# Optimization experiments

Measured on AMD Instinct MI355X. Metric: run time of the kernel, lower is better.

Reference implementation:

```python
import jax, jax.numpy as jnp
import numpy as np
from jax import lax

B, T, E, D, A, C, FILT = 32, 1600, 1024, 1024, 512, 10, 100
SCALING = 2.0


def setup_inputs() -> dict:
    key = jax.random.key(0)
    ks = jax.random.split(key, 14)
    enc_hs_pad = jax.random.normal(ks[0], (B, T, E), dtype=jnp.float32)
    # lengths in [T//2, T] so every row has valid positions
    enc_hs_len = jax.random.randint(ks[1], (B,), T // 2, T + 1, dtype=jnp.int32)
    dec_z = jax.random.normal(ks[2], (B, D), dtype=jnp.float32)
    # previous attention weights: uniform over valid frames, normalized
    valid = (jnp.arange(T)[None, :] < enc_hs_len[:, None]).astype(jnp.float32)
    raw = jax.random.uniform(ks[3], (B, T), dtype=jnp.float32) * valid
    att_prev = raw / jnp.sum(raw, axis=1, keepdims=True)
    att_h = 0.1 * jax.random.normal(ks[4], (B, A), dtype=jnp.float32)
    att_c = 0.1 * jax.random.normal(ks[5], (B, A), dtype=jnp.float32)
    W_enc = jax.random.normal(ks[6], (A, E), dtype=jnp.float32) / np.sqrt(E)
    b_enc = jax.random.normal(ks[7], (A,), dtype=jnp.float32) * 0.01
    W_dec = jax.random.normal(ks[8], (A, D), dtype=jnp.float32) / np.sqrt(D)
    conv_w = jax.random.normal(ks[9], (C, 1, 2 * FILT + 1), dtype=jnp.float32) / np.sqrt(2 * FILT + 1)
    W_ih = jax.random.normal(ks[10], (4 * A, C), dtype=jnp.float32) / np.sqrt(C)
    W_hh = jax.random.normal(ks[11], (4 * A, A), dtype=jnp.float32) / np.sqrt(A)
    W_g = jax.random.normal(ks[12], (A,), dtype=jnp.float32) / np.sqrt(A)
    b_g = jnp.zeros((1,), dtype=jnp.float32)
    return {"enc_hs_pad": enc_hs_pad, "enc_hs_len": enc_hs_len, "dec_z": dec_z,
            "att_prev": att_prev, "att_h": att_h, "att_c": att_c,
            "W_enc": W_enc, "b_enc": b_enc, "W_dec": W_dec, "conv_w": conv_w,
            "W_ih": W_ih, "W_hh": W_hh, "W_g": W_g, "b_g": b_g}


def reference(enc_hs_pad, enc_hs_len, dec_z, att_prev, att_h, att_c,
              W_enc, b_enc, W_dec, conv_w, W_ih, W_hh, W_g, b_g):
    t_len = enc_hs_pad.shape[1]
    filts = (conv_w.shape[-1] - 1) // 2

    # precompute encoder projection (B, T, A)
    pre_enc = jnp.einsum('bte,ae->bta', enc_hs_pad, W_enc) + b_enc

    # location conv on previous attention: (B,1,T) -> (B,C,T), relu, global max-pool over T
    att_conv = lax.conv_general_dilated(att_prev[:, None, :], conv_w,
                                        window_strides=(1,), padding=[(filts, filts)],
                                        dimension_numbers=('NCH', 'OIH', 'NCH'))
    att_feat = jnp.max(jax.nn.relu(att_conv), axis=-1)  # (B, C)

    # LSTMCell (no bias), pytorch gate order i, f, g, o
    gates = att_feat @ W_ih.T + att_h @ W_hh.T  # (B, 4A)
    i, f, g, o = jnp.split(gates, 4, axis=-1)
    c_new = jax.nn.sigmoid(f) * att_c + jax.nn.sigmoid(i) * jnp.tanh(g)
    h_new = jax.nn.sigmoid(o) * jnp.tanh(c_new)  # (B, A)

    dec_proj = dec_z @ W_dec.T  # (B, A)
    # scores (B, T)
    e = jnp.tanh(h_new[:, None, :] + pre_enc + dec_proj[:, None, :]) @ W_g + b_g

    mask = jnp.arange(t_len)[None, :] >= enc_hs_len[:, None]  # True = pad
    e = jnp.where(mask, jnp.finfo(e.dtype).min, e)
    w = jax.nn.softmax(SCALING * e, axis=1)  # (B, T)

    ctx = jnp.einsum('bt,bte->be', w, enc_hs_pad)  # (B, E)
    return ctx, w, h_new, c_new
```

## Files before the change

kernel.cpp:

```cpp
#include <hip/hip_runtime.h>
#include <hip/hip_bf16.h>

#define BB 32
#define TT 1600
#define EE 1024
#define AA 512
#define CC 10
#define KW 201

typedef __attribute__((ext_vector_type(8))) short short8;
typedef __attribute__((ext_vector_type(4))) float f32x4;

__device__ __forceinline__ float sigm(float x) { return 1.f / (1.f + expf(-x)); }

__device__ __forceinline__ unsigned int cvt2(float a, float b) {
    float2 f2; f2.x = a; f2.y = b;
    __hip_bfloat162 h = __float22bfloat162_rn(f2);
    unsigned int r;
    __builtin_memcpy(&r, &h, 4);
    return r;
}

__device__ __forceinline__ void gl_lds16(const void* g, void* l) {
    __builtin_amdgcn_global_load_lds(
        (const __attribute__((address_space(1))) unsigned int*)g,
        (__attribute__((address_space(3))) unsigned int*)l, 16, 0, 0);
}

#define AF_OFF   0
#define R_OFF    320
#define E_OFF    16704
#define WBF_OFF  67904

#define CTX_OFF 0
#define W_OFF   32768
#define H_OFF   83968
#define C_OFF   100352

__global__ void prep_kernel(const float* __restrict__ att_prev,
                            const float* __restrict__ conv_w,
                            const float* __restrict__ W_enc,
                            float* __restrict__ af,
                            unsigned short* __restrict__ Wbf) {
    int bx = blockIdx.x, tid = threadIdx.x;
    if (bx >= 320) {
        int i = (bx - 320) * 256 + tid;
        float4 v = reinterpret_cast<const float4*>(W_enc)[i];
        uint2 p;
        p.x = cvt2(v.x, v.y);
        p.y = cvt2(v.z, v.w);
        reinterpret_cast<uint2*>(Wbf)[i] = p;
        return;
    }
    int b = bx / 10, c = bx % 10;
    __shared__ float xs[1808];
    __shared__ float wsm[KW];
    __shared__ float red[256];
    const float* xp = att_prev + b * TT;
    for (int i = tid; i < 1808; i += 256) {
        int g = i - 100;
        xs[i] = (g >= 0 && g < TT) ? xp[g] : 0.f;
    }
    if (tid < KW) wsm[tid] = conv_w[c * KW + tid];
    __syncthreads();
    float mx = 0.f;
    #pragma unroll 1
    for (int sweep = 0; sweep < 2; ++sweep) {
        int t0 = sweep * 1024 + tid * 4;
        if (t0 >= TT) break;
        float a0 = xs[t0], a1 = xs[t0 + 1], a2 = xs[t0 + 2], a3 = xs[t0 + 3];
        float s0 = 0.f, s1 = 0.f, s2 = 0.f, s3 = 0.f;
        #pragma unroll 4
        for (int k = 0; k < KW; ++k) {
            float w = wsm[k];
            s0 += w * a0; s1 += w * a1; s2 += w * a2; s3 += w * a3;
            a0 = a1; a1 = a2; a2 = a3;
            a3 = xs[t0 + k + 4];
        }
        mx = fmaxf(mx, fmaxf(fmaxf(s0, s1), fmaxf(s2, s3)));
    }
    red[tid] = mx; __syncthreads();
    for (int s = 128; s > 0; s >>= 1) {
        if (tid < s) red[tid] = fmaxf(red[tid], red[tid + s]);
        __syncthreads();
    }
    if (tid == 0) af[b * CC + c] = red[0];
}

__global__ void gates_lstm_kernel(const float* __restrict__ af,
                                  const float* __restrict__ att_h,
                                  const float* __restrict__ dec_z,
                                  const float* __restrict__ att_c,
                                  const float* __restrict__ W_ih,
                                  const float* __restrict__ W_hh,
                                  const float* __restrict__ W_dec,
                                  float* __restrict__ out,
                                  float* __restrict__ r_ws) {
    __shared__ float gsm[8][32];
    __shared__ float dsm[8][32];
    int tid = threadIdx.x;
    int a0 = blockIdx.x * 2;
    int b = tid & 31;
    if (tid < 256) {
        int u = tid >> 5;
        int gate = u >> 1, ai = u & 1;
        int j = gate * 512 + a0 + ai;
        float s = 0.f;
        #pragma unroll
        for (int k = 0; k < 10; ++k) s += af[b * 10 + k] * W_ih[j * 10 + k];
        const float4* wr = reinterpret_cast<const float4*>(W_hh + (size_t)j * 512);
        const float4* hr = reinterpret_cast<const float4*>(att_h + b * 512);
        #pragma unroll 4
        for (int k = 0; k < 128; ++k) {
            float4 w = wr[k], h = hr[k];
            s += w.x * h.x + w.y * h.y + w.z * h.z + w.w * h.w;
        }
        gsm[u][b] = s;
    } else {
        int v = (tid - 256) >> 5;
        int ai = v & 1, q = v >> 1;
        int a = a0 + ai;
        const float4* wr = reinterpret_cast<const float4*>(W_dec + (size_t)a * 1024) + q * 64;
        const float4* zr = reinterpret_cast<const float4*>(dec_z + (size_t)b * 1024) + q * 64;
        float s = 0.f;
        #pragma unroll 4
        for (int k = 0; k < 64; ++k) {
            float4 w = wr[k], z = zr[k];
            s += w.x * z.x + w.y * z.y + w.z * z.z + w.w * z.w;
        }
        dsm[v][b] = s;
    }
    __syncthreads();
    if (tid < 64) {
        int ai = tid >> 5;
        int a = a0 + ai;
        float ig = gsm[ai][b], fg = gsm[2 + ai][b], gg = gsm[4 + ai][b], og = gsm[6 + ai][b];
        float cn = sigm(fg) * att_c[b * 512 + a] + sigm(ig) * tanhf(gg);
        float hn = sigm(og) * tanhf(cn);
        out[H_OFF + b * 512 + a] = hn;
        out[C_OFF + b * 512 + a] = cn;
        float dec = dsm[ai][b] + dsm[2 + ai][b] + dsm[4 + ai][b] + dsm[6 + ai][b];
        r_ws[b * 512 + a] = hn + dec;
    }
}

__global__ void __launch_bounds__(1024, 4)
score_gemm_kernel(const float* __restrict__ enc,
                  const unsigned short* __restrict__ Wbf,
                  const float* __restrict__ b_enc,
                  const float* __restrict__ r_ws,
                  const float* __restrict__ W_g,
                  float* __restrict__ e_ws) {
    __shared__ __align__(16) short As[2][4096];
    __shared__ __align__(16) short Bs[2][8192];
    __shared__ float e_part[8][128];

    int tid = threadIdx.x;
    int lane = tid & 63, wv = tid >> 6;
    int wm = wv >> 3, wn = wv & 7;
    int col = lane & 15, quad = lane >> 4;
    int m0 = blockIdx.x * 128;

    const unsigned short* bsrc = Wbf + (size_t)((tid >> 6) * 16 + (tid & 15)) * EE
                                 + ((tid >> 4) & 3) * 8;
    int arow = tid >> 3, akq2 = tid & 7;
    const float* asrc = enc + (size_t)(m0 + arow) * EE + akq2 * 4;
    int adst = (arow >> 4) * 512 + ((akq2 >> 1) * 16 + (arow & 15)) * 8 + (akq2 & 1) * 4;

    f32x4 acc[4][2][2];
    #pragma unroll
    for (int mt = 0; mt < 4; ++mt)
        #pragma unroll
        for (int h = 0; h < 2; ++h)
            #pragma unroll
            for (int nt = 0; nt < 2; ++nt)
                acc[mt][h][nt] = (f32x4){0.f, 0.f, 0.f, 0.f};

    {
        gl_lds16(bsrc, &Bs[0][tid * 8]);
        float4 v = *reinterpret_cast<const float4*>(asrc);
        uint2 p; p.x = cvt2(v.x, v.y); p.y = cvt2(v.z, v.w);
        *reinterpret_cast<uint2*>(&As[0][adst]) = p;
    }
    __syncthreads();

    int bufA = 0;
    for (int k0 = 0; k0 < EE; k0 += 32) {
        bool last = (k0 == EE - 32);
        gl_lds16(bsrc + (size_t)256 * EE + k0, &Bs[1][tid * 8]);
        short8 a_frag[4];
        #pragma unroll
        for (int mt = 0; mt < 4; ++mt)
            a_frag[mt] = *reinterpret_cast<const short8*>(
                &As[bufA][(wm * 4 + mt) * 512 + (quad * 16 + col) * 8]);
        #pragma unroll
        for (int nt = 0; nt < 2; ++nt) {
            short8 bf = *reinterpret_cast<const short8*>(
                &Bs[0][(wn * 2 + nt) * 512 + (quad * 16 + col) * 8]);
            #pragma unroll
            for (int mt = 0; mt < 4; ++mt)
                acc[mt][0][nt] = __builtin_amdgcn_mfma_f32_16x16x32_bf16(
                    a_frag[mt], bf, acc[mt][0][nt], 0, 0, 0);
        }
        __syncthreads();
        float4 av;
        if (!last) {
            av = *reinterpret_cast<const float4*>(asrc + k0 + 32);
            gl_lds16(bsrc + k0 + 32, &Bs[0][tid * 8]);
        }
        #pragma unroll
        for (int nt = 0; nt < 2; ++nt) {
            short8 bf = *reinterpret_cast<const short8*>(
                &Bs[1][(wn * 2 + nt) * 512 + (quad * 16 + col) * 8]);
            #pragma unroll
            for (int mt = 0; mt < 4; ++mt)
                acc[mt][1][nt] = __builtin_amdgcn_mfma_f32_16x16x32_bf16(
                    a_frag[mt], bf, acc[mt][1][nt], 0, 0, 0);
        }
        if (!last) {
            uint2 p; p.x = cvt2(av.x, av.y); p.y = cvt2(av.z, av.w);
            *reinterpret_cast<uint2*>(&As[bufA ^ 1][adst]) = p;
        }
        __syncthreads();
        bufA ^= 1;
    }

    float wg[2][2], bn[2][2];
    #pragma unroll
    for (int h = 0; h < 2; ++h)
        #pragma unroll
        for (int nt = 0; nt < 2; ++nt) {
            int n = h * 256 + wn * 32 + nt * 16 + col;
            wg[h][nt] = W_g[n];
            bn[h][nt] = b_enc[n];
        }
    #pragma unroll
    for (int mt = 0; mt < 4; ++mt) {
        int mg = m0 + wm * 64 + mt * 16;
        int bb = mg / TT;
        float rr[2][2];
        #pragma unroll
        for (int h = 0; h < 2; ++h)
            #pragma unroll
            for (int nt = 0; nt < 2; ++nt)
                rr[h][nt] = r_ws[bb * AA + h * 256 + wn * 32 + nt * 16 + col];
        #pragma unroll
        for (int reg = 0; reg < 4; ++reg) {
            float p = 0.f;
            #pragma unroll
            for (int h = 0; h < 2; ++h)
                #pragma unroll
                for (int nt = 0; nt < 2; ++nt)
                    p += wg[h][nt] * tanhf(acc[mt][h][nt][reg] + bn[h][nt] + rr[h][nt]);
            p += __shfl_xor(p, 1);
            p += __shfl_xor(p, 2);
            p += __shfl_xor(p, 4);
            p += __shfl_xor(p, 8);
            if (col == 0) e_part[wn][wm * 64 + mt * 16 + quad * 4 + reg] = p;
        }
    }
    __syncthreads();
    if (tid < 128) {
        float s = 0.f;
        #pragma unroll
        for (int i = 0; i < 8; ++i) s += e_part[i][tid];
        e_ws[m0 + tid] = s;
    }
}

__global__ void ctx_softmax_kernel(const float* __restrict__ enc,
                                   const float* __restrict__ e_ws,
                                   const int* __restrict__ lens,
                                   float* __restrict__ w_out,
                                   float* __restrict__ ctx) {
    int b = blockIdx.x, ch = blockIdx.y;
    int tid = threadIdx.x;
    __shared__ float w_sm[1600];
    __shared__ float red[512];
    __shared__ float part[8][128];
    int len = lens[b];
    const float* e = e_ws + b * TT;
    float mx = -3.4e38f;
    for (int t = tid; t < len; t += 512) mx = fmaxf(mx, e[t]);
    red[tid] = mx; __syncthreads();
    for (int s = 256; s > 0; s >>= 1) {
        if (tid < s) red[tid] = fmaxf(red[tid], red[tid + s]);
        __syncthreads();
    }
    mx = red[0]; __syncthreads();
    float sum = 0.f;
    for (int t = tid; t < TT; t += 512) {
        float p = (t < len) ? expf(2.f * (e[t] - mx)) : 0.f;
        w_sm[t] = p; sum += p;
    }
    red[tid] = sum; __syncthreads();
    for (int s = 256; s > 0; s >>= 1) {
        if (tid < s) red[tid] += red[tid + s];
        __syncthreads();
    }
    float inv = 1.f / red[0];
    __syncthreads();
    for (int t = tid; t < TT; t += 512) {
        float wv = w_sm[t] * inv;
        w_sm[t] = wv;
        if (ch == 0) w_out[b * TT + t] = wv;
    }
    __syncthreads();
    int lane2 = tid & 63, w8 = tid >> 6;
    int tb = w8 * 200;
    const float* base = enc + (size_t)(b * TT + tb) * EE + ch * 128 + lane2 * 2;
    float cx = 0.f, cy = 0.f;
    #pragma unroll 1
    for (int i = 0; i < 200; i += 8) {
        #pragma unroll
        for (int j = 0; j < 8; ++j) {
            float2 v = *reinterpret_cast<const float2*>(base + (size_t)(i + j) * EE);
            float ww = w_sm[tb + i + j];
            cx += ww * v.x; cy += ww * v.y;
        }
    }
    part[w8][lane2 * 2] = cx;
    part[w8][lane2 * 2 + 1] = cy;
    __syncthreads();
    if (tid < 128) {
        float s = 0.f;
        #pragma unroll
        for (int i = 0; i < 8; ++i) s += part[i][tid];
        ctx[b * EE + ch * 128 + tid] = s;
    }
}

extern "C" void kernel_launch(void* const* d_in, const int* in_sizes, int n_in,
                              void* d_out, int out_size, void* d_ws, size_t ws_size,
                              hipStream_t stream) {
    const float* enc      = (const float*)d_in[0];
    const int*   lens     = (const int*)d_in[1];
    const float* dec_z    = (const float*)d_in[2];
    const float* att_prev = (const float*)d_in[3];
    const float* att_h    = (const float*)d_in[4];
    const float* att_c    = (const float*)d_in[5];
    const float* W_enc    = (const float*)d_in[6];
    const float* b_enc    = (const float*)d_in[7];
    const float* W_dec    = (const float*)d_in[8];
    const float* conv_w   = (const float*)d_in[9];
    const float* W_ih     = (const float*)d_in[10];
    const float* W_hh     = (const float*)d_in[11];
    const float* W_g      = (const float*)d_in[12];

    float* out = (float*)d_out;
    float* ws  = (float*)d_ws;
    float* af   = ws + AF_OFF;
    float* r_ws = ws + R_OFF;
    float* e_ws = ws + E_OFF;
    unsigned short* Wbf = (unsigned short*)(ws + WBF_OFF);

    prep_kernel<<<832, 256, 0, stream>>>(att_prev, conv_w, W_enc, af, Wbf);
    gates_lstm_kernel<<<256, 512, 0, stream>>>(af, att_h, dec_z, att_c,
                                               W_ih, W_hh, W_dec, out, r_ws);
    score_gemm_kernel<<<400, 1024, 0, stream>>>(enc, Wbf, b_enc, r_ws, W_g, e_ws);
    ctx_softmax_kernel<<<dim3(BB, 8), 512, 0, stream>>>(enc, e_ws, lens,
                                                        out + W_OFF, out + CTX_OFF);
}
```

Baseline: 494.4 us.

## Load W_enc fragments directly from global into registers, drop LDS B staging

The score GEMM no longer stages the bf16 W_enc tile in shared memory through global_load_lds. Each wave now reads its B fragments straight from global/L2 into registers, and only the A tile stays double-buffered in LDS. The loop is unrolled into explicit chunks that prefetch A two steps ahead, raise wave priority around the MFMA block, and use one barrier per step instead of two. This removes LDS traffic and a barrier per iteration, but W_enc is now re-read from cache by every wave, and any global latency is exposed to the MFMAs since B has no prefetch.

```diff
diff --git a/kernel.cpp b/kernel.cpp
--- a/kernel.cpp
+++ b/kernel.cpp
@@ -19,12 +19,6 @@
     unsigned int r;
     __builtin_memcpy(&r, &h, 4);
     return r;
-}
-
-__device__ __forceinline__ void gl_lds16(const void* g, void* l) {
-    __builtin_amdgcn_global_load_lds(
-        (const __attribute__((address_space(1))) unsigned int*)g,
-        (__attribute__((address_space(3))) unsigned int*)l, 16, 0, 0);
 }
 
 #define AF_OFF   0
@@ -152,7 +146,6 @@
                   const float* __restrict__ W_g,
                   float* __restrict__ e_ws) {
     __shared__ __align__(16) short As[2][4096];
-    __shared__ __align__(16) short Bs[2][8192];
     __shared__ float e_part[8][128];
 
     int tid = threadIdx.x;
@@ -161,11 +154,16 @@
     int col = lane & 15, quad = lane >> 4;
     int m0 = blockIdx.x * 128;
 
-    const unsigned short* bsrc = Wbf + (size_t)((tid >> 6) * 16 + (tid & 15)) * EE
-                                 + ((tid >> 4) & 3) * 8;
     int arow = tid >> 3, akq2 = tid & 7;
     const float* asrc = enc + (size_t)(m0 + arow) * EE + akq2 * 4;
     int adst = (arow >> 4) * 512 + ((akq2 >> 1) * 16 + (arow & 15)) * 8 + (akq2 & 1) * 4;
+
+    const unsigned short* bp[2][2];
+    #pragma unroll
+    for (int h = 0; h < 2; ++h)
+        #pragma unroll
+        for (int nt = 0; nt < 2; ++nt)
+            bp[h][nt] = Wbf + (size_t)(h * 256 + wn * 32 + nt * 16 + col) * EE + quad * 8;
 
     f32x4 acc[4][2][2];
     #pragma unroll
@@ -176,54 +174,65 @@
             for (int nt = 0; nt < 2; ++nt)
                 acc[mt][h][nt] = (f32x4){0.f, 0.f, 0.f, 0.f};
 
+    float4 av0, av1;
     {
-        gl_lds16(bsrc, &Bs[0][tid * 8]);
-        float4 v = *reinterpret_cast<const float4*>(asrc);
-        uint2 p; p.x = cvt2(v.x, v.y); p.y = cvt2(v.z, v.w);
-        *reinterpret_cast<uint2*>(&As[0][adst]) = p;
-    }
-    __syncthreads();
-
-    int bufA = 0;
-    for (int k0 = 0; k0 < EE; k0 += 32) {
-        bool last = (k0 == EE - 32);
-        gl_lds16(bsrc + (size_t)256 * EE + k0, &Bs[1][tid * 8]);
-        short8 a_frag[4];
-        #pragma unroll
-        for (int mt = 0; mt < 4; ++mt)
-            a_frag[mt] = *reinterpret_cast<const short8*>(
-                &As[bufA][(wm * 4 + mt) * 512 + (quad * 16 + col) * 8]);
-        #pragma unroll
-        for (int nt = 0; nt < 2; ++nt) {
-            short8 bf = *reinterpret_cast<const short8*>(
-                &Bs[0][(wn * 2 + nt) * 512 + (quad * 16 + col) * 8]);
-            #pragma unroll
-            for (int mt = 0; mt < 4; ++mt)
-                acc[mt][0][nt] = __builtin_amdgcn_mfma_f32_16x16x32_bf16(
-                    a_frag[mt], bf, acc[mt][0][nt], 0, 0, 0);
-        }
-        __syncthreads();
-        float4 av;
-        if (!last) {
-            av = *reinterpret_cast<const float4*>(asrc + k0 + 32);
-            gl_lds16(bsrc + k0 + 32, &Bs[0][tid * 8]);
-        }
-        #pragma unroll
-        for (int nt = 0; nt < 2; ++nt) {
-            short8 bf = *reinterpret_cast<const short8*>(
-                &Bs[1][(wn * 2 + nt) * 512 + (quad * 16 + col) * 8]);
-            #pragma unroll
-            for (int mt = 0; mt < 4; ++mt)
-                acc[mt][1][nt] = __builtin_amdgcn_mfma_f32_16x16x32_bf16(
-                    a_frag[mt], bf, acc[mt][1][nt], 0, 0, 0);
-        }
-        if (!last) {
-            uint2 p; p.x = cvt2(av.x, av.y); p.y = cvt2(av.z, av.w);
-            *reinterpret_cast<uint2*>(&As[bufA ^ 1][adst]) = p;
-        }
-        __syncthreads();
-        bufA ^= 1;
-    }
+        float4 p = *reinterpret_cast<const float4*>(asrc);
+        av1 = *reinterpret_cast<const float4*>(asrc + 32);
+        uint2 q; q.x = cvt2(p.x, p.y); q.y = cvt2(p.z, p.w);
+        *reinterpret_cast<uint2*>(&As[0][adst]) = q;
+        asm volatile("s_waitcnt lgkmcnt(0)\n\ts_barrier" ::: "memory");
+    }
+
+#define SCORE_CHUNK(RB, AVC, AVI, KC, PREF, WR)                                        \
+    {                                                                                  \
+        int k0 = (KC) * 32;                                                            \
+        short8 bf00 = *reinterpret_cast<const short8*>(bp[0][0] + k0);                 \
+        short8 bf01 = *reinterpret_cast<const short8*>(bp[0][1] + k0);                 \
+        short8 bf10 = *reinterpret_cast<const short8*>(bp[1][0] + k0);                 \
+        short8 bf11 = *reinterpret_cast<const short8*>(bp[1][1] + k0);                 \
+        if (PREF)                                                                      \
+            AVI = *reinterpret_cast<const float4*>(asrc + ((KC) + 2) * 32);            \
+        short8 af0 = *reinterpret_cast<const short8*>(                                 \
+            &As[RB][(wm * 4 + 0) * 512 + (quad * 16 + col) * 8]);                      \
+        short8 af1 = *reinterpret_cast<const short8*>(                                 \
+            &As[RB][(wm * 4 + 1) * 512 + (quad * 16 + col) * 8]);                      \
+        short8 af2 = *reinterpret_cast<const short8*>(                                 \
+            &As[RB][(wm * 4 + 2) * 512 + (quad * 16 + col) * 8]);                      \
+        short8 af3 = *reinterpret_cast<const short8*>(                                 \
+            &As[RB][(wm * 4 + 3) * 512 + (quad * 16 + col) * 8]);                      \
+        __builtin_amdgcn_s_setprio(1);                                                 \
+        acc[0][0][0] = __builtin_amdgcn_mfma_f32_16x16x32_bf16(af0, bf00, acc[0][0][0], 0, 0, 0); \
+        acc[0][0][1] = __builtin_amdgcn_mfma_f32_16x16x32_bf16(af0, bf01, acc[0][0][1], 0, 0, 0); \
+        acc[0][1][0] = __builtin_amdgcn_mfma_f32_16x16x32_bf16(af0, bf10, acc[0][1][0], 0, 0, 0); \
+        acc[0][1][1] = __builtin_amdgcn_mfma_f32_16x16x32_bf16(af0, bf11, acc[0][1][1], 0, 0, 0); \
+        acc[1][0][0] = __builtin_amdgcn_mfma_f32_16x16x32_bf16(af1, bf00, acc[1][0][0], 0, 0, 0); \
+        acc[1][0][1] = __builtin_amdgcn_mfma_f32_16x16x32_bf16(af1, bf01, acc[1][0][1], 0, 0, 0); \
+        acc[1][1][0] = __builtin_amdgcn_mfma_f32_16x16x32_bf16(af1, bf10, acc[1][1][0], 0, 0, 0); \
+        acc[1][1][1] = __builtin_amdgcn_mfma_f32_16x16x32_bf16(af1, bf11, acc[1][1][1], 0, 0, 0); \
+        acc[2][0][0] = __builtin_amdgcn_mfma_f32_16x16x32_bf16(af2, bf00, acc[2][0][0], 0, 0, 0); \
+        acc[2][0][1] = __builtin_amdgcn_mfma_f32_16x16x32_bf16(af2, bf01, acc[2][0][1], 0, 0, 0); \
+        acc[2][1][0] = __builtin_amdgcn_mfma_f32_16x16x32_bf16(af2, bf10, acc[2][1][0], 0, 0, 0); \
+        acc[2][1][1] = __builtin_amdgcn_mfma_f32_16x16x32_bf16(af2, bf11, acc[2][1][1], 0, 0, 0); \
+        acc[3][0][0] = __builtin_amdgcn_mfma_f32_16x16x32_bf16(af3, bf00, acc[3][0][0], 0, 0, 0); \
+        acc[3][0][1] = __builtin_amdgcn_mfma_f32_16x16x32_bf16(af3, bf01, acc[3][0][1], 0, 0, 0); \
+        acc[3][1][0] = __builtin_amdgcn_mfma_f32_16x16x32_bf16(af3, bf10, acc[3][1][0], 0, 0, 0); \
+        acc[3][1][1] = __builtin_amdgcn_mfma_f32_16x16x32_bf16(af3, bf11, acc[3][1][1], 0, 0, 0); \
+        __builtin_amdgcn_s_setprio(0);                                                 \
+        if (WR) {                                                                      \
+            uint2 q; q.x = cvt2(AVC.x, AVC.y); q.y = cvt2(AVC.z, AVC.w);               \
+            *reinterpret_cast<uint2*>(&As[(RB) ^ 1][adst]) = q;                        \
+        }                                                                              \
+        asm volatile("s_waitcnt lgkmcnt(0)\n\ts_barrier" ::: "memory");                \
+    }
+
+    #pragma unroll 1
+    for (int c = 0; c < 30; c += 2) {
+        SCORE_CHUNK(0, av1, av0, c, 1, 1)
+        SCORE_CHUNK(1, av0, av1, c + 1, 1, 1)
+    }
+    SCORE_CHUNK(0, av1, av0, 30, 0, 1)
+    SCORE_CHUNK(1, av0, av1, 31, 0, 0)
+#undef SCORE_CHUNK
 
     float wg[2][2], bn[2][2];
     #pragma unroll
```

After: 545.4 us. 10.3% more time.

## Triple-buffer score GEMM with async fp32 A loads into swizzled LDS

Applied to the files above, without the earlier changes.

Rewrites the score GEMM main loop as a three-stage pipeline. Both the fp32 encoder tile and the bf16 weight tile are fetched with asynchronous global-to-LDS loads, the A tile uses an XOR-swizzled layout, and fp32-to-bf16 conversion moves to the point where fragments are read. The loop computes both N halves per K chunk and uses explicit vmcnt waits plus s_setprio around the MFMA burst. This is meant to hide global load latency and cut the register staging and conversion work that sat on the critical path. The cost is about 144KB of LDS per block, which likely limits each CU to a single block.

```diff
diff --git a/kernel.cpp b/kernel.cpp
--- a/kernel.cpp
+++ b/kernel.cpp
@@ -151,8 +151,8 @@
                   const float* __restrict__ r_ws,
                   const float* __restrict__ W_g,
                   float* __restrict__ e_ws) {
-    __shared__ __align__(16) short As[2][4096];
-    __shared__ __align__(16) short Bs[2][8192];
+    __shared__ __align__(16) short Bs[3][16384];
+    __shared__ __align__(16) char  AsB[3][16384];
     __shared__ float e_part[8][128];
 
     int tid = threadIdx.x;
@@ -161,11 +161,22 @@
     int col = lane & 15, quad = lane >> 4;
     int m0 = blockIdx.x * 128;
 
-    const unsigned short* bsrc = Wbf + (size_t)((tid >> 6) * 16 + (tid & 15)) * EE
-                                 + ((tid >> 4) & 3) * 8;
-    int arow = tid >> 3, akq2 = tid & 7;
-    const float* asrc = enc + (size_t)(m0 + arow) * EE + akq2 * 4;
-    int adst = (arow >> 4) * 512 + ((akq2 >> 1) * 16 + (arow & 15)) * 8 + (akq2 & 1) * 4;
+    int agrp = tid >> 7;
+    int P = tid & 127;
+    int Lc = P ^ ((P >> 3) & 7);
+    int as_ = Lc >> 1, asub = Lc & 1;
+    int akoct = as_ >> 4, arowin = as_ & 15;
+    const float* asrc = enc + (size_t)(m0 + agrp * 16 + arowin) * EE + akoct * 8 + asub * 4;
+
+    int L0 = (quad * 16 + col) * 2;
+    int L1 = L0 + 1;
+    int p0 = (L0 ^ ((L0 >> 3) & 7)) * 16;
+    int p1 = (L1 ^ ((L1 >> 3) & 7)) * 16;
+
+    int bslot = tid & 63;
+    int boct = bslot >> 4, brow = bslot & 15;
+    const unsigned short* bsrc0 = Wbf + (size_t)((tid >> 6) * 16 + brow) * EE + boct * 8;
+    const unsigned short* bsrc1 = Wbf + (size_t)(((tid >> 6) + 16) * 16 + brow) * EE + boct * 8;
 
     f32x4 acc[4][2][2];
     #pragma unroll
@@ -176,63 +187,74 @@
             for (int nt = 0; nt < 2; ++nt)
                 acc[mt][h][nt] = (f32x4){0.f, 0.f, 0.f, 0.f};
 
-    {
-        gl_lds16(bsrc, &Bs[0][tid * 8]);
-        float4 v = *reinterpret_cast<const float4*>(asrc);
-        uint2 p; p.x = cvt2(v.x, v.y); p.y = cvt2(v.z, v.w);
-        *reinterpret_cast<uint2*>(&As[0][adst]) = p;
-    }
-    __syncthreads();
-
-    int bufA = 0;
-    for (int k0 = 0; k0 < EE; k0 += 32) {
-        bool last = (k0 == EE - 32);
-        gl_lds16(bsrc + (size_t)256 * EE + k0, &Bs[1][tid * 8]);
-        short8 a_frag[4];
-        #pragma unroll
-        for (int mt = 0; mt < 4; ++mt)
-            a_frag[mt] = *reinterpret_cast<const short8*>(
-                &As[bufA][(wm * 4 + mt) * 512 + (quad * 16 + col) * 8]);
-        #pragma unroll
-        for (int nt = 0; nt < 2; ++nt) {
-            short8 bf = *reinterpret_cast<const short8*>(
-                &Bs[0][(wn * 2 + nt) * 512 + (quad * 16 + col) * 8]);
-            #pragma unroll
-            for (int mt = 0; mt < 4; ++mt)
-                acc[mt][0][nt] = __builtin_amdgcn_mfma_f32_16x16x32_bf16(
-                    a_frag[mt], bf, acc[mt][0][nt], 0, 0, 0);
-        }
-        __syncthreads();
-        float4 av;
-        if (!last) {
-            av = *reinterpret_cast<const float4*>(asrc + k0 + 32);
-            gl_lds16(bsrc + k0 + 32, &Bs[0][tid * 8]);
-        }
-        #pragma unroll
-        for (int nt = 0; nt < 2; ++nt) {
-            short8 bf = *reinterpret_cast<const short8*>(
-                &Bs[1][(wn * 2 + nt) * 512 + (quad * 16 + col) * 8]);
-            #pragma unroll
-            for (int mt = 0; mt < 4; ++mt)
-                acc[mt][1][nt] = __builtin_amdgcn_mfma_f32_16x16x32_bf16(
-                    a_frag[mt], bf, acc[mt][1][nt], 0, 0, 0);
-        }
-        if (!last) {
-            uint2 p; p.x = cvt2(av.x, av.y); p.y = cvt2(av.z, av.w);
-            *reinterpret_cast<uint2*>(&As[bufA ^ 1][adst]) = p;
-        }
-        __syncthreads();
-        bufA ^= 1;
-    }
-
-    float wg[2][2], bn[2][2];
+    gl_lds16(asrc,              &AsB[0][tid * 16]);
+    gl_lds16(bsrc0,             &Bs[0][tid * 8]);
+    gl_lds16(bsrc1,             &Bs[0][8192 + tid * 8]);
+    gl_lds16(asrc + 32,         &AsB[1][tid * 16]);
+    gl_lds16(bsrc0 + 32,        &Bs[1][tid * 8]);
+    gl_lds16(bsrc1 + 32,        &Bs[1][8192 + tid * 8]);
+    asm volatile("s_waitcnt vmcnt(3)" ::: "memory");
+    __builtin_amdgcn_s_barrier();
+
+#define SCORE_CHUNK(KC, RB, SB, STAGE, SYNC, WN)                                \
+    {                                                                           \
+        if (STAGE) {                                                            \
+            gl_lds16(asrc + ((KC) + 2) * 32,  &AsB[SB][tid * 16]);              \
+            gl_lds16(bsrc0 + ((KC) + 2) * 32, &Bs[SB][tid * 8]);                \
+            gl_lds16(bsrc1 + ((KC) + 2) * 32, &Bs[SB][8192 + tid * 8]);         \
+        }                                                                       \
+        short8 af[4];                                                           \
+        _Pragma("unroll")                                                       \
+        for (int mt = 0; mt < 4; ++mt) {                                        \
+            const char* ab = &AsB[RB][(wm * 4 + mt) * 2048];                    \
+            float4 x = *reinterpret_cast<const float4*>(ab + p0);               \
+            float4 y = *reinterpret_cast<const float4*>(ab + p1);               \
+            union { short8 s; unsigned int u[4]; } cv;                          \
+            cv.u[0] = cvt2(x.x, x.y); cv.u[1] = cvt2(x.z, x.w);                 \
+            cv.u[2] = cvt2(y.x, y.y); cv.u[3] = cvt2(y.z, y.w);                 \
+            af[mt] = cv.s;                                                      \
+        }                                                                       \
+        short8 bf[2][2];                                                        \
+        _Pragma("unroll")                                                       \
+        for (int h = 0; h < 2; ++h)                                             \
+            _Pragma("unroll")                                                   \
+            for (int nt = 0; nt < 2; ++nt)                                      \
+                bf[h][nt] = *reinterpret_cast<const short8*>(                   \
+                    &Bs[RB][(h * 16 + wn * 2 + nt) * 512 + (quad * 16 + col) * 8]); \
+        __builtin_amdgcn_s_setprio(1);                                          \
+        _Pragma("unroll")                                                       \
+        for (int mt = 0; mt < 4; ++mt)                                          \
+            _Pragma("unroll")                                                   \
+            for (int h = 0; h < 2; ++h)                                         \
+                _Pragma("unroll")                                               \
+                for (int nt = 0; nt < 2; ++nt)                                  \
+                    acc[mt][h][nt] = __builtin_amdgcn_mfma_f32_16x16x32_bf16(   \
+                        af[mt], bf[h][nt], acc[mt][h][nt], 0, 0, 0);            \
+        __builtin_amdgcn_s_setprio(0);                                          \
+        if (SYNC) {                                                             \
+            asm volatile("s_waitcnt vmcnt(" #WN ")" ::: "memory");              \
+            __builtin_amdgcn_s_barrier();                                       \
+        }                                                                       \
+    }
+
+    #pragma unroll 1
+    for (int c = 0; c < 30; c += 3) {
+        SCORE_CHUNK(c,     0, 2, 1, 1, 3)
+        SCORE_CHUNK(c + 1, 1, 0, 1, 1, 3)
+        SCORE_CHUNK(c + 2, 2, 1, 1, 1, 3)
+    }
+    SCORE_CHUNK(30, 0, 0, 0, 1, 0)
+    SCORE_CHUNK(31, 1, 0, 0, 0, 0)
+#undef SCORE_CHUNK
+
+    float wg[2][2], bn_[2][2];
     #pragma unroll
     for (int h = 0; h < 2; ++h)
         #pragma unroll
         for (int nt = 0; nt < 2; ++nt) {
             int n = h * 256 + wn * 32 + nt * 16 + col;
             wg[h][nt] = W_g[n];
-            bn[h][nt] = b_enc[n];
+            bn_[h][nt] = b_enc[n];
         }
     #pragma unroll
     for (int mt = 0; mt < 4; ++mt) {
@@ -251,7 +273,7 @@
             for (int h = 0; h < 2; ++h)
                 #pragma unroll
                 for (int nt = 0; nt < 2; ++nt)
-                    p += wg[h][nt] * tanhf(acc[mt][h][nt][reg] + bn[h][nt] + rr[h][nt]);
+                    p += wg[h][nt] * tanhf(acc[mt][h][nt][reg] + bn_[h][nt] + rr[h][nt]);
             p += __shfl_xor(p, 1);
             p += __shfl_xor(p, 2);
             p += __shfl_xor(p, 4);
```

Result: faster. 481.6 us (-2.6%).

## Split score GEMM over attention halves with async fp32 A-tile staging

Applied to the files above, without the earlier changes.

The score GEMM now runs twice as many 512-thread blocks. Each block covers 128 rows and half of the attention dimension, and writes a partial score into a second workspace slice that the softmax kernel sums. The fp32 encoder tile is loaded straight into LDS with global_load_lds and converted to bf16 when fragments are read, replacing the register round-trip. It also adds a simple double-buffered stage with MFMA priority hints. In exchange the encoder is read twice from global memory, the kernel uses more LDS, and the bf16 conversion work is repeated per wave.

```diff
diff --git a/kernel.cpp b/kernel.cpp
--- a/kernel.cpp
+++ b/kernel.cpp
@@ -30,7 +30,7 @@
 #define AF_OFF   0
 #define R_OFF    320
 #define E_OFF    16704
-#define WBF_OFF  67904
+#define WBF_OFF  119104
 
 #define CTX_OFF 0
 #define W_OFF   32768
@@ -144,114 +144,102 @@
     }
 }
 
-__global__ void __launch_bounds__(1024, 4)
+__global__ void __launch_bounds__(512, 4)
 score_gemm_kernel(const float* __restrict__ enc,
                   const unsigned short* __restrict__ Wbf,
                   const float* __restrict__ b_enc,
                   const float* __restrict__ r_ws,
                   const float* __restrict__ W_g,
                   float* __restrict__ e_ws) {
-    __shared__ __align__(16) short As[2][4096];
     __shared__ __align__(16) short Bs[2][8192];
-    __shared__ float e_part[8][128];
+    __shared__ __align__(16) float Af[2][4096];
 
     int tid = threadIdx.x;
     int lane = tid & 63, wv = tid >> 6;
-    int wm = wv >> 3, wn = wv & 7;
+    int wm = wv >> 2, wn = wv & 3;
     int col = lane & 15, quad = lane >> 4;
-    int m0 = blockIdx.x * 128;
-
-    const unsigned short* bsrc = Wbf + (size_t)((tid >> 6) * 16 + (tid & 15)) * EE
-                                 + ((tid >> 4) & 3) * 8;
-    int arow = tid >> 3, akq2 = tid & 7;
-    const float* asrc = enc + (size_t)(m0 + arow) * EE + akq2 * 4;
-    int adst = (arow >> 4) * 512 + ((akq2 >> 1) * 16 + (arow & 15)) * 8 + (akq2 & 1) * 4;
-
-    f32x4 acc[4][2][2];
+    int mblk = blockIdx.x >> 1, cb = blockIdx.x & 1;
+    int m0 = mblk * 128;
+
+    const float* asrc0 = enc + (size_t)(m0 + (tid >> 7) * 16 + (tid & 15)) * EE
+                             + ((tid & 127) >> 4) * 4;
+    const float* asrc1 = asrc0 + (size_t)64 * EE;
+    const unsigned short* bsrc0 = Wbf + (size_t)(cb * 256 + (tid >> 6) * 16 + (tid & 15)) * EE
+                                      + ((tid & 63) >> 4) * 8;
+    const unsigned short* bsrc1 = bsrc0 + (size_t)128 * EE;
+
+    f32x4 acc[4][4];
     #pragma unroll
     for (int mt = 0; mt < 4; ++mt)
         #pragma unroll
-        for (int h = 0; h < 2; ++h)
+        for (int nt = 0; nt < 4; ++nt)
+            acc[mt][nt] = (f32x4){0.f, 0.f, 0.f, 0.f};
+
+#define STAGE(KC, BUF)                                                          \
+    {                                                                           \
+        gl_lds16(asrc0 + (KC) * 32, (char*)Af[BUF] + tid * 16);                 \
+        gl_lds16(asrc1 + (KC) * 32, (char*)Af[BUF] + 8192 + tid * 16);          \
+        gl_lds16(bsrc0 + (KC) * 32, (char*)Bs[BUF] + tid * 16);                 \
+        gl_lds16(bsrc1 + (KC) * 32, (char*)Bs[BUF] + 8192 + tid * 16);          \
+    }
+
+    STAGE(0, 0)
+    __syncthreads();
+
+    #pragma unroll 2
+    for (int c = 0; c < 32; ++c) {
+        int buf = c & 1;
+        if (c < 31) STAGE(c + 1, buf ^ 1)
+        short8 afr[4];
+        #pragma unroll
+        for (int mt = 0; mt < 4; ++mt) {
+            const float* ap = Af[buf] + (wm * 4 + mt) * 512;
+            float4 x = *reinterpret_cast<const float4*>(ap + quad * 128 + col * 4);
+            float4 y = *reinterpret_cast<const float4*>(ap + quad * 128 + col * 4 + 64);
+            union { short8 s; unsigned int u[4]; } cv;
+            cv.u[0] = cvt2(x.x, x.y); cv.u[1] = cvt2(x.z, x.w);
+            cv.u[2] = cvt2(y.x, y.y); cv.u[3] = cvt2(y.z, y.w);
+            afr[mt] = cv.s;
+        }
+        short8 bfr[4];
+        #pragma unroll
+        for (int nt = 0; nt < 4; ++nt)
+            bfr[nt] = *reinterpret_cast<const short8*>(
+                &Bs[buf][(wn * 4 + nt) * 512 + (quad * 16 + col) * 8]);
+        __builtin_amdgcn_s_setprio(1);
+        #pragma unroll
+        for (int mt = 0; mt < 4; ++mt)
             #pragma unroll
-            for (int nt = 0; nt < 2; ++nt)
-                acc[mt][h][nt] = (f32x4){0.f, 0.f, 0.f, 0.f};
-
-    {
-        gl_lds16(bsrc, &Bs[0][tid * 8]);
-        float4 v = *reinterpret_cast<const float4*>(asrc);
-        uint2 p; p.x = cvt2(v.x, v.y); p.y = cvt2(v.z, v.w);
-        *reinterpret_cast<uint2*>(&As[0][adst]) = p;
-    }
-    __syncthreads();
-
-    int bufA = 0;
-    for (int k0 = 0; k0 < EE; k0 += 32) {
-        bool last = (k0 == EE - 32);
-        gl_lds16(bsrc + (size_t)256 * EE + k0, &Bs[1][tid * 8]);
-        short8 a_frag[4];
-        #pragma unroll
-        for (int mt = 0; mt < 4; ++mt)
-            a_frag[mt] = *reinterpret_cast<const short8*>(
-                &As[bufA][(wm * 4 + mt) * 512 + (quad * 16 + col) * 8]);
-        #pragma unroll
-        for (int nt = 0; nt < 2; ++nt) {
-            short8 bf = *reinterpret_cast<const short8*>(
-                &Bs[0][(wn * 2 + nt) * 512 + (quad * 16 + col) * 8]);
-            #pragma unroll
-            for (int mt = 0; mt < 4; ++mt)
-                acc[mt][0][nt] = __builtin_amdgcn_mfma_f32_16x16x32_bf16(
-                    a_frag[mt], bf, acc[mt][0][nt], 0, 0, 0);
-        }
+            for (int nt = 0; nt < 4; ++nt)
+                acc[mt][nt] = __builtin_amdgcn_mfma_f32_16x16x32_bf16(
+                    afr[mt], bfr[nt], acc[mt][nt], 0, 0, 0);
+        __builtin_amdgcn_s_setprio(0);
         __syncthreads();
-        float4 av;
-        if (!last) {
-            av = *reinterpret_cast<const float4*>(asrc + k0 + 32);
-            gl_lds16(bsrc + k0 + 32, &Bs[0][tid * 8]);
-        }
-        #pragma unroll
-        for (int nt = 0; nt < 2; ++nt) {
-            short8 bf = *reinterpret_cast<const short8*>(
-                &Bs[1][(wn * 2 + nt) * 512 + (quad * 16 + col) * 8]);
-            #pragma unroll
-            for (int mt = 0; mt < 4; ++mt)
-                acc[mt][1][nt] = __builtin_amdgcn_mfma_f32_16x16x32_bf16(
-                    a_frag[mt], bf, acc[mt][1][nt], 0, 0, 0);
-        }
-        if (!last) {
-            uint2 p; p.x = cvt2(av.x, av.y); p.y = cvt2(av.z, av.w);
-            *reinterpret_cast<uint2*>(&As[bufA ^ 1][adst]) = p;
-        }
-        __syncthreads();
-        bufA ^= 1;
-    }
-
-    float wg[2][2], bn[2][2];
+    }
+#undef STAGE
+
+    float (*e_part)[128] = reinterpret_cast<float (*)[128]>(&Af[0][0]);
+    float wg[4], bn_[4];
     #pragma unroll
-    for (int h = 0; h < 2; ++h)
-        #pragma unroll
-        for (int nt = 0; nt < 2; ++nt) {
-            int n = h * 256 + wn * 32 + nt * 16 + col;
-            wg[h][nt] = W_g[n];
-            bn[h][nt] = b_enc[n];
-        }
+    for (int nt = 0; nt < 4; ++nt) {
+        int n = cb * 256 + wn * 64 + nt * 16 + col;
+        wg[nt] = W_g[n];
+        bn_[nt] = b_enc[n];
+    }
     #pragma unroll
     for (int mt = 0; mt < 4; ++mt) {
         int mg = m0 + wm * 64 + mt * 16;
         int bb = mg / TT;
-        float rr[2][2];
-        #pragma unroll
-        for (int h = 0; h < 2; ++h)
-            #pragma unroll
-            for (int nt = 0; nt < 2; ++nt)
-                rr[h][nt] = r_ws[bb * AA + h * 256 + wn * 32 + nt * 16 + col];
+        float rr[4];
+        #pragma unroll
+        for (int nt = 0; nt < 4; ++nt)
+            rr[nt] = r_ws[bb * AA + cb * 256 + wn * 64 + nt * 16 + col];
         #pragma unroll
         for (int reg = 0; reg < 4; ++reg) {
             float p = 0.f;
             #pragma unroll
-            for (int h = 0; h < 2; ++h)
-                #pragma unroll
-                for (int nt = 0; nt < 2; ++nt)
-                    p += wg[h][nt] * tanhf(acc[mt][h][nt][reg] + bn[h][nt] + rr[h][nt]);
+            for (int nt = 0; nt < 4; ++nt)
+                p += wg[nt] * tanhf(acc[mt][nt][reg] + bn_[nt] + rr[nt]);
             p += __shfl_xor(p, 1);
             p += __shfl_xor(p, 2);
             p += __shfl_xor(p, 4);
@@ -261,10 +249,8 @@
     }
     __syncthreads();
     if (tid < 128) {
-        float s = 0.f;
-        #pragma unroll
-        for (int i = 0; i < 8; ++i) s += e_part[i][tid];
-        e_ws[m0 + tid] = s;
+        float s = e_part[0][tid] + e_part[1][tid] + e_part[2][tid] + e_part[3][tid];
+        e_ws[cb * 51200 + m0 + tid] = s;
     }
 }
 
@@ -279,9 +265,10 @@
     __shared__ float red[512];
     __shared__ float part[8][128];
     int len = lens[b];
-    const float* e = e_ws + b * TT;
+    const float* e0 = e_ws + b * TT;
+    const float* e1 = e_ws + 51200 + b * TT;
     float mx = -3.4e38f;
-    for (int t = tid; t < len; t += 512) mx = fmaxf(mx, e[t]);
+    for (int t = tid; t < len; t += 512) mx = fmaxf(mx, e0[t] + e1[t]);
     red[tid] = mx; __syncthreads();
     for (int s = 256; s > 0; s >>= 1) {
         if (tid < s) red[tid] = fmaxf(red[tid], red[tid + s]);
@@ -290,7 +277,7 @@
     mx = red[0]; __syncthreads();
     float sum = 0.f;
     for (int t = tid; t < TT; t += 512) {
-        float p = (t < len) ? expf(2.f * (e[t] - mx)) : 0.f;
+        float p = (t < len) ? expf(2.f * (e0[t] + e1[t] - mx)) : 0.f;
         w_sm[t] = p; sum += p;
     }
     red[tid] = sum; __syncthreads();
@@ -357,7 +344,7 @@
     prep_kernel<<<832, 256, 0, stream>>>(att_prev, conv_w, W_enc, af, Wbf);
     gates_lstm_kernel<<<256, 512, 0, stream>>>(af, att_h, dec_z, att_c,
                                                W_ih, W_hh, W_dec, out, r_ws);
-    score_gemm_kernel<<<400, 1024, 0, stream>>>(enc, Wbf, b_enc, r_ws, W_g, e_ws);
+    score_gemm_kernel<<<800, 512, 0, stream>>>(enc, Wbf, b_enc, r_ws, W_g, e_ws);
     ctx_softmax_kernel<<<dim3(BB, 8), 512, 0, stream>>>(enc, e_ws, lens,
                                                         out + W_OFF, out + CTX_OFF);
 }
```

After: 497.5 us. About the same (+0.6%).
